# Kernel tuning notes

Hardware: AMD Instinct MI355X
Metric: run time of the kernel (lower is better)

## Reference

```python
import jax, jax.numpy as jnp
import numpy as np

B, S = 1, 2048
H, KV, D = 32, 8, 128          # query heads, kv heads, head_size
G = H // KV                     # num_queries_per_kv (GQA group size)
SCALE = 1.0 / float(np.sqrt(D))


def setup_inputs() -> dict:
    key = jax.random.key(0)
    k1, k2, k3 = jax.random.split(key, 3)
    slopes = jnp.asarray(2.0 ** (-8.0 * np.arange(1, H + 1) / H), dtype=jnp.float32)
    return {
        "query": jax.random.normal(k1, (B, S, H * D), dtype=jnp.float32),
        "key": jax.random.normal(k2, (B, S, KV * D), dtype=jnp.float32),
        "value": jax.random.normal(k3, (B, S, KV * D), dtype=jnp.float32),
        "alibi_slopes": slopes,
    }


def reference(query, key, value, alibi_slopes):
    b, s, _ = query.shape
    # [B,S,H*D] -> [B,KV,G,S,D] (GQA unflatten of query heads into kv groups)
    q = query.reshape(b, s, KV, G, D).transpose(0, 2, 3, 1, 4)
    k = key.reshape(b, s, KV, D).transpose(0, 2, 1, 3)      # [B,KV,S,D]
    v = value.reshape(b, s, KV, D).transpose(0, 2, 1, 3)    # [B,KV,S,D]

    # _make_alibi_bias: bias[i,j] = (j - i) * slope_h, then unflatten heads to (KV, G)
    pos = jnp.arange(s)
    rel = (pos[None, :] - pos[:, None]).astype(query.dtype)         # [S,S]
    bias = alibi_slopes[:, None, None] * rel                        # [H,S,S]
    causal = jnp.where(pos[None, :] > pos[:, None], -jnp.inf, 0.0).astype(query.dtype)
    bias = (bias + causal).reshape(KV, G, s, s)                     # [KV,G,S,S]

    # scaled QK^T + bias, softmax, AV (non-fused prompt_attention path)
    scores = jnp.einsum('bkgsd,bktd->bkgst', q * SCALE, k) + bias   # [B,KV,G,S,S]
    probs = jax.nn.softmax(scores, axis=-1)
    out = jnp.einsum('bkgst,bktd->bkgsd', probs, v)                 # [B,KV,G,S,D]
    # flatten (KV,G) -> H and back to [B,S,H*D]
    return out.transpose(0, 3, 1, 2, 4).reshape(b, s, H * D)
```

## Files before the change

kernel.cpp:

```cpp
#include <hip/hip_runtime.h>
#include <hip/hip_bf16.h>

#define S_LEN 2048
#define NHEADS 32
#define NKV 8
#define HD 128
#define QK_SCALE 0.08838834764831845f
#define LOG2E 1.4426950408889634f
#define QK_SCALE2 (QK_SCALE * LOG2E)
#define DTHR 11.5416f

#define BQ 128
#define BK 32
#define NQT (S_LEN / BQ)
#define QSTR (NHEADS * HD)
#define KSTR (NKV * HD)

#define K_STRIDE 136
#define VT_STRIDE 40
#define P_STRIDE 40

typedef __attribute__((ext_vector_type(8))) short bf16x8;
typedef __attribute__((ext_vector_type(4))) float f32x4;
typedef __attribute__((ext_vector_type(4))) unsigned u32x4;
typedef __attribute__((ext_vector_type(2))) unsigned u32x2;

__device__ inline unsigned cvt_pk_bf16(float lo, float hi) {
    unsigned r;
    asm("v_cvt_pk_bf16_f32 %0, %1, %2" : "=v"(r) : "v"(lo), "v"(hi));
    return r;
}
__device__ inline bf16x8 as_bf16x8(u32x4 v) {
    union { u32x4 u; bf16x8 b; } c; c.u = v; return c.b;
}

__global__ __launch_bounds__(512) void attn_fwd(
    const float* __restrict__ Q, const float* __restrict__ K,
    const float* __restrict__ V, const float* __restrict__ SL,
    float* __restrict__ O)
{
    const int bx   = blockIdx.x;
    const int h    = bx & (NHEADS - 1);
    const int qt   = (NQT - 1) - (bx >> 5);
    const int kvh  = h >> 2;
    const float slope  = SL[h];
    const float slope2 = slope * LOG2E;

    const int tid  = threadIdx.x;
    const int w    = tid >> 6;
    const int lane = tid & 63;
    const int l16  = lane & 15;
    const int lq   = lane >> 4;

    __shared__ short Ks[2][BK * K_STRIDE];
    __shared__ short VTs[2][HD * VT_STRIDE];
    __shared__ short Ps[8][16 * P_STRIDE];

    const int qrow0 = qt * BQ + w * 16;
    const int q     = qrow0 + l16;

    bf16x8 qf[4];
    {
        const float* qp = Q + (size_t)q * QSTR + h * HD + lq * 8;
        #pragma unroll
        for (int d0 = 0; d0 < 4; ++d0) {
            f32x4 a = *(const f32x4*)(qp + d0 * 32);
            f32x4 b = *(const f32x4*)(qp + d0 * 32 + 4);
            u32x4 t;
            t[0] = cvt_pk_bf16(a[0] * QK_SCALE2, a[1] * QK_SCALE2);
            t[1] = cvt_pk_bf16(a[2] * QK_SCALE2, a[3] * QK_SCALE2);
            t[2] = cvt_pk_bf16(b[0] * QK_SCALE2, b[1] * QK_SCALE2);
            t[3] = cvt_pk_bf16(b[2] * QK_SCALE2, b[3] * QK_SCALE2);
            qf[d0] = as_bf16x8(t);
        }
    }

    f32x4 acc[8];
    #pragma unroll
    for (int t = 0; t < 8; ++t) acc[t] = (f32x4){0.f, 0.f, 0.f, 0.f};
    float m_ = -1e30f, l_ = 0.f;

    const int kv_end = qt * BQ + BQ;
    int kb_start = 0;
    {
        float th = (float)(qt * BQ) - 31.0f - 45.0f / slope;
        int t = (int)floorf(th);
        kb_start = (t < 0) ? 0 : (((t >> 5) + 1) << 5);
    }

    const int sr  = tid >> 4, scc = tid & 15;
    const int vd  = tid & 127;
    const int vrb = (tid >> 7) * 8;
    const float* Kbase = K + (size_t)kvh * HD + scc * 8;
    const float* Vbase = V + (size_t)kvh * HD + vd;

    float kr[8], vr[8];

    auto load_regs = [&](int kb) {
        const float* kp = Kbase + (size_t)(kb + sr) * KSTR;
        *(f32x4*)&kr[0] = *(const f32x4*)kp;
        *(f32x4*)&kr[4] = *(const f32x4*)(kp + 4);
        #pragma unroll
        for (int j = 0; j < 8; ++j)
            vr[j] = Vbase[(size_t)(kb + vrb + j) * KSTR];
    };

    auto store_tile = [&](int b) {
        u32x4 t;
        t[0] = cvt_pk_bf16(kr[0], kr[1]);
        t[1] = cvt_pk_bf16(kr[2], kr[3]);
        t[2] = cvt_pk_bf16(kr[4], kr[5]);
        t[3] = cvt_pk_bf16(kr[6], kr[7]);
        *(u32x4*)&Ks[b][sr * K_STRIDE + scc * 8] = t;
        t[0] = cvt_pk_bf16(vr[0], vr[1]);
        t[1] = cvt_pk_bf16(vr[2], vr[3]);
        t[2] = cvt_pk_bf16(vr[4], vr[5]);
        t[3] = cvt_pk_bf16(vr[6], vr[7]);
        *(u32x4*)&VTs[b][vd * VT_STRIDE + vrb] = t;
    };

    load_regs(kb_start);
    store_tile(0);
    int cur = 0;

    for (int kb = kb_start; kb < kv_end; kb += BK) {
        asm volatile("s_waitcnt lgkmcnt(0)\n\ts_barrier" ::: "memory");

        const bool has_next = (kb + BK) < kv_end;
        if (has_next) load_regs(kb + BK);

        const bool live = (kb <= qrow0 + 15) &&
                          (slope * (float)(qrow0 - kb - 31) < 45.0f);
        if (live) {
            const short* Kc = &Ks[cur][0];
            const short* Vc = &VTs[cur][0];

            f32x4 sc0 = (f32x4){0.f,0.f,0.f,0.f};
            f32x4 sc1 = (f32x4){0.f,0.f,0.f,0.f};
            #pragma unroll
            for (int d0 = 0; d0 < 4; ++d0) {
                bf16x8 kf0 = *(const bf16x8*)&Kc[l16 * K_STRIDE + d0 * 32 + lq * 8];
                bf16x8 kf1 = *(const bf16x8*)&Kc[(16 + l16) * K_STRIDE + d0 * 32 + lq * 8];
                sc0 = __builtin_amdgcn_mfma_f32_16x16x32_bf16(kf0, qf[d0], sc0, 0, 0, 0);
                sc1 = __builtin_amdgcn_mfma_f32_16x16x32_bf16(kf1, qf[d0], sc1, 0, 0, 0);
            }

            const int kq0 = kb + 4 * lq - q;
            float s[8];
            #pragma unroll
            for (int i = 0; i < 4; ++i) {
                int d0i = kq0 + i, d1i = kq0 + 16 + i;
                float b0 = __builtin_fmaf(slope2, (float)d0i, sc0[i]);
                float b1 = __builtin_fmaf(slope2, (float)d1i, sc1[i]);
                s[i]     = (d0i > 0) ? -1e30f : b0;
                s[i + 4] = (d1i > 0) ? -1e30f : b1;
            }

            float rm = fmaxf(fmaxf(fmaxf(s[0], s[1]), fmaxf(s[2], s[3])),
                             fmaxf(fmaxf(s[4], s[5]), fmaxf(s[6], s[7])));
            rm = fmaxf(rm, __shfl_xor(rm, 16));
            rm = fmaxf(rm, __shfl_xor(rm, 32));

            bool need = (rm > m_ + DTHR);
            if (__any(need)) {
                float mn    = need ? rm : m_;
                float alpha = exp2f(m_ - mn);
                m_ = mn;
                l_ *= alpha;
                #pragma unroll
                for (int t = 0; t < 8; ++t) {
                    acc[t][0] *= alpha; acc[t][1] *= alpha;
                    acc[t][2] *= alpha; acc[t][3] *= alpha;
                }
            }

            float p[8];
            #pragma unroll
            for (int j = 0; j < 8; ++j) p[j] = exp2f(s[j] - m_);
            float ts = ((p[0] + p[1]) + (p[2] + p[3])) +
                       ((p[4] + p[5]) + (p[6] + p[7]));
            ts += __shfl_xor(ts, 16);
            ts += __shfl_xor(ts, 32);
            l_ += ts;

            u32x2 pa, pb;
            pa[0] = cvt_pk_bf16(p[0], p[1]); pa[1] = cvt_pk_bf16(p[2], p[3]);
            pb[0] = cvt_pk_bf16(p[4], p[5]); pb[1] = cvt_pk_bf16(p[6], p[7]);

            short* PsW = &Ps[w][0];
            *(u32x2*)&PsW[l16 * P_STRIDE + 4 * lq]      = pa;
            *(u32x2*)&PsW[l16 * P_STRIDE + 16 + 4 * lq] = pb;
            asm volatile("s_waitcnt lgkmcnt(0)" ::: "memory");
            bf16x8 pf = *(const bf16x8*)&PsW[l16 * P_STRIDE + lq * 8];

            #pragma unroll
            for (int nt = 0; nt < 8; ++nt) {
                bf16x8 vf = *(const bf16x8*)&Vc[(nt * 16 + l16) * VT_STRIDE + lq * 8];
                acc[nt] = __builtin_amdgcn_mfma_f32_16x16x32_bf16(vf, pf, acc[nt], 0, 0, 0);
            }
        }

        if (has_next) store_tile(cur ^ 1);
        cur ^= 1;
    }

    {
        float rl = 1.0f / l_;
        float* op = O + (size_t)q * QSTR + h * HD + 4 * lq;
        #pragma unroll
        for (int nt = 0; nt < 8; ++nt) {
            f32x4 o = acc[nt];
            o[0] *= rl; o[1] *= rl; o[2] *= rl; o[3] *= rl;
            *(f32x4*)(op + nt * 16) = o;
        }
    }
}

extern "C" void kernel_launch(void* const* d_in, const int* in_sizes, int n_in,
                              void* d_out, int out_size, void* d_ws, size_t ws_size,
                              hipStream_t stream) {
    const float* Q  = (const float*)d_in[0];
    const float* K  = (const float*)d_in[1];
    const float* V  = (const float*)d_in[2];
    const float* SL = (const float*)d_in[3];
    float* O = (float*)d_out;

    dim3 grid(NQT * NHEADS);
    dim3 block(512);
    attn_fwd<<<grid, block, 0, stream>>>(Q, K, V, SL, O);
}
```

Measured before the change: 103.1 us.

## Split long ALiBi KV windows across two blocks with a combine kernel

Tiles whose KV window exceeds a threshold are now processed by two blocks, each covering half the KV range. Each block writes its unnormalized accumulator and running max and sum to workspace, and a second kernel merges them with log-sum-exp weights. This targets load imbalance from heads with small slopes, whose long windows form the critical path. It costs workspace traffic, an extra launch, and idle early-exit blocks in a grid twice the size.

Measured after the change: 118.3 us. 14.8% more time.

```diff
diff --git a/kernel.cpp b/kernel.cpp
--- a/kernel.cpp
+++ b/kernel.cpp
@@ -20,6 +20,11 @@
 #define VT_STRIDE 40
 #define P_STRIDE 40
 
+#define SPLIT_THRESH 1024
+#define NSLOT 512
+#define SLOT_ACC 16384
+#define SLOT_ML 256
+
 typedef __attribute__((ext_vector_type(8))) short bf16x8;
 typedef __attribute__((ext_vector_type(4))) float f32x4;
 typedef __attribute__((ext_vector_type(4))) unsigned u32x4;
@@ -34,17 +39,35 @@
     union { u32x4 u; bf16x8 b; } c; c.u = v; return c.b;
 }
 
+__device__ inline int alibi_start(int qt, float slope) {
+    float th = (float)(qt * BQ) - 31.0f - 45.0f / slope;
+    int t = (int)floorf(th);
+    return (t < 0) ? 0 : (((t >> 5) + 1) << 5);
+}
+
 __global__ __launch_bounds__(512) void attn_fwd(
     const float* __restrict__ Q, const float* __restrict__ K,
     const float* __restrict__ V, const float* __restrict__ SL,
-    float* __restrict__ O)
+    float* __restrict__ O, float* __restrict__ ws_acc,
+    float* __restrict__ ws_ml, int split_ok)
 {
     const int bx   = blockIdx.x;
-    const int h    = bx & (NHEADS - 1);
-    const int qt   = (NQT - 1) - (bx >> 5);
+    const int c    = bx & 1;
+    const int h    = (bx >> 1) & (NHEADS - 1);
+    const int qt   = (NQT - 1) - (bx >> 6);
     const int kvh  = h >> 2;
     const float slope  = SL[h];
     const float slope2 = slope * LOG2E;
+
+    const int kv_end   = qt * BQ + BQ;
+    const int kb_start = alibi_start(qt, slope);
+    const int window   = kv_end - kb_start;
+    const int nu       = (split_ok && window > SPLIT_THRESH) ? 2 : 1;
+    if (c >= nu) return;
+    int clen = window;
+    if (nu == 2) clen = (((window + 1) >> 1) + 31) & ~31;
+    const int kb0 = kb_start + c * clen;
+    int kb1 = kb0 + clen; if (kb1 > kv_end) kb1 = kv_end;
 
     const int tid  = threadIdx.x;
     const int w    = tid >> 6;
@@ -80,14 +103,6 @@
     for (int t = 0; t < 8; ++t) acc[t] = (f32x4){0.f, 0.f, 0.f, 0.f};
     float m_ = -1e30f, l_ = 0.f;
 
-    const int kv_end = qt * BQ + BQ;
-    int kb_start = 0;
-    {
-        float th = (float)(qt * BQ) - 31.0f - 45.0f / slope;
-        int t = (int)floorf(th);
-        kb_start = (t < 0) ? 0 : (((t >> 5) + 1) << 5);
-    }
-
     const int sr  = tid >> 4, scc = tid & 15;
     const int vd  = tid & 127;
     const int vrb = (tid >> 7) * 8;
@@ -119,14 +134,14 @@
         *(u32x4*)&VTs[b][vd * VT_STRIDE + vrb] = t;
     };
 
-    load_regs(kb_start);
+    load_regs(kb0);
     store_tile(0);
     int cur = 0;
 
-    for (int kb = kb_start; kb < kv_end; kb += BK) {
+    for (int kb = kb0; kb < kb1; kb += BK) {
         asm volatile("s_waitcnt lgkmcnt(0)\n\ts_barrier" ::: "memory");
 
-        const bool has_next = (kb + BK) < kv_end;
+        const bool has_next = (kb + BK) < kb1;
         if (has_next) load_regs(kb + BK);
 
         const bool live = (kb <= qrow0 + 15) &&
@@ -204,7 +219,7 @@
         cur ^= 1;
     }
 
-    {
+    if (nu == 1) {
         float rl = 1.0f / l_;
         float* op = O + (size_t)q * QSTR + h * HD + 4 * lq;
         #pragma unroll
@@ -213,6 +228,59 @@
             o[0] *= rl; o[1] *= rl; o[2] *= rl; o[3] *= rl;
             *(f32x4*)(op + nt * 16) = o;
         }
+    } else {
+        const int slot = ((qt - 8) * NHEADS + h) * 2 + c;
+        const int rloc = w * 16 + l16;
+        float* pr = ws_acc + (size_t)slot * SLOT_ACC + (size_t)rloc * HD + 4 * lq;
+        #pragma unroll
+        for (int nt = 0; nt < 8; ++nt)
+            *(f32x4*)(pr + nt * 16) = acc[nt];
+        if (lq == 0) {
+            float* ml = ws_ml + (size_t)slot * SLOT_ML + rloc * 2;
+            ml[0] = m_; ml[1] = l_;
+        }
+    }
+}
+
+__global__ __launch_bounds__(256) void attn_combine(
+    const float* __restrict__ SL, const float* __restrict__ ws_acc,
+    const float* __restrict__ ws_ml, float* __restrict__ O)
+{
+    const int bx = blockIdx.x;
+    const int h  = bx & (NHEADS - 1);
+    const int qt = 8 + (bx >> 5);
+    const float slope = SL[h];
+
+    const int kv_end   = qt * BQ + BQ;
+    const int kb_start = alibi_start(qt, slope);
+    if (kv_end - kb_start <= SPLIT_THRESH) return;
+
+    const int tid = threadIdx.x;
+    const int r   = tid >> 1;
+    const int dh  = (tid & 1) * 64;
+
+    const int slot0 = ((qt - 8) * NHEADS + h) * 2;
+    const float* ml0 = ws_ml + (size_t)slot0 * SLOT_ML + r * 2;
+    const float* ml1 = ws_ml + (size_t)(slot0 + 1) * SLOT_ML + r * 2;
+    float m0 = ml0[0], l0 = ml0[1];
+    float m1 = ml1[0], l1 = ml1[1];
+    float M  = fmaxf(m0, m1);
+    float w0 = exp2f(m0 - M), w1 = exp2f(m1 - M);
+    float inv = 1.0f / (w0 * l0 + w1 * l1);
+
+    const float* a0 = ws_acc + (size_t)slot0 * SLOT_ACC + (size_t)r * HD + dh;
+    const float* a1 = a0 + SLOT_ACC;
+    float* op = O + (size_t)(qt * BQ + r) * QSTR + h * HD + dh;
+    #pragma unroll
+    for (int j = 0; j < 16; ++j) {
+        f32x4 x0 = *(const f32x4*)(a0 + 4 * j);
+        f32x4 x1 = *(const f32x4*)(a1 + 4 * j);
+        f32x4 o;
+        o[0] = (w0 * x0[0] + w1 * x1[0]) * inv;
+        o[1] = (w0 * x0[1] + w1 * x1[1]) * inv;
+        o[2] = (w0 * x0[2] + w1 * x1[2]) * inv;
+        o[3] = (w0 * x0[3] + w1 * x1[3]) * inv;
+        *(f32x4*)(op + 4 * j) = o;
     }
 }
 
@@ -225,7 +293,15 @@
     const float* SL = (const float*)d_in[3];
     float* O = (float*)d_out;
 
-    dim3 grid(NQT * NHEADS);
-    dim3 block(512);
-    attn_fwd<<<grid, block, 0, stream>>>(Q, K, V, SL, O);
-}
+    const size_t needed = ((size_t)NSLOT * SLOT_ACC + (size_t)NSLOT * SLOT_ML)
+                          * sizeof(float);
+    const int split_ok = (d_ws != nullptr && ws_size >= needed) ? 1 : 0;
+    float* ws_acc = (float*)d_ws;
+    float* ws_ml  = ws_acc + (size_t)NSLOT * SLOT_ACC;
+
+    attn_fwd<<<dim3(NQT * NHEADS * 2), dim3(512), 0, stream>>>(
+        Q, K, V, SL, O, ws_acc, ws_ml, split_ok);
+    if (split_ok)
+        attn_combine<<<dim3(8 * NHEADS), dim3(256), 0, stream>>>(
+            SL, ws_acc, ws_ml, O);
+}
```
